# Performance work log

Hardware: AMD Instinct MI355X
Metric: run time of the kernel (lower is better)

The kernel has to match this reference:

```python
import jax, jax.numpy as jnp
import numpy as np

B, S, D, NH = 2, 2048, 2048, 16
HD = D // NH  # 128


def setup_inputs() -> dict:
    key = jax.random.key(0)
    ks = jax.random.split(key, 7)
    s = 1.0 / np.sqrt(D)
    return {
        "hidden_states": jax.random.normal(ks[0], (B, S, D), dtype=jnp.float32),
        "Wq": jax.random.normal(ks[1], (D, D), dtype=jnp.float32) * s,
        "Wk": jax.random.normal(ks[2], (D, D), dtype=jnp.float32) * s,
        "Wv": jax.random.normal(ks[3], (D, D), dtype=jnp.float32) * s,
        "Wo": jax.random.normal(ks[4], (D, D), dtype=jnp.float32) * s,
        # phase projections: hidden -> num_heads (zero-init in the module; use small
        # random values so the phase path is numerically exercised)
        "Wpq": jax.random.normal(ks[5], (D, NH), dtype=jnp.float32) * 0.02,
        "Wpk": jax.random.normal(ks[6], (D, NH), dtype=jnp.float32) * 0.02,
    }


def reference(hidden_states, Wq, Wk, Wv, Wo, Wpq, Wpk):
    x = hidden_states  # [B,S,D]
    # ---- base_attn: standard causal multi-head self-attention ----
    q = (x @ Wq).reshape(B, S, NH, HD).transpose(0, 2, 1, 3)  # [B,H,S,hd]
    k = (x @ Wk).reshape(B, S, NH, HD).transpose(0, 2, 1, 3)
    v = (x @ Wv).reshape(B, S, NH, HD).transpose(0, 2, 1, 3)
    scores = jnp.einsum("bhqd,bhkd->bhqk", q, k) / np.sqrt(HD)  # [B,H,S,S]
    causal = jnp.tril(jnp.ones((S, S), dtype=bool))
    scores = jnp.where(causal, scores, jnp.float32(-1e9))
    probs = jax.nn.softmax(scores, axis=-1)
    ctx = jnp.einsum("bhqk,bhkd->bhqd", probs, v)  # [B,H,S,hd]
    attn_output = ctx.transpose(0, 2, 1, 3).reshape(B, S, D) @ Wo  # [B,S,D]
    # ---- phase modulation ----
    # original: cos(pq[b,q,None,h] - pk[b,None,k,h]).mean(dims=(k,h))  -> [B,S]
    # identity: cos(a-b) = cos a * cos b + sin a * sin b lets us avoid the
    # [B,S,S,H] tensor; the math is identical.
    pq = x @ Wpq  # [B,S,H]
    pk = x @ Wpk  # [B,S,H]
    Ck = jnp.cos(pk).sum(axis=1)  # [B,H]
    Sk = jnp.sin(pk).sum(axis=1)  # [B,H]
    phase_mod = (jnp.cos(pq) * Ck[:, None, :] + jnp.sin(pq) * Sk[:, None, :]).sum(-1) / (S * NH)  # [B,S]
    return attn_output * (1.0 + 0.1 * phase_mod[..., None])
```

## Files before the change

kernel.cpp:

```cpp
#include <hip/hip_runtime.h>
#include <hip/hip_bf16.h>

typedef __attribute__((ext_vector_type(8))) short short8;
typedef __attribute__((ext_vector_type(4))) float f32x4;
typedef __attribute__((ext_vector_type(16))) float f32x16;
typedef __attribute__((ext_vector_type(4))) int i32x4;
typedef unsigned short u16;

#define S_LEN 2048
#define D_DIM 2048
#define NHEAD 16
#define HDIM 128
#define M_ROWS 4096

#define MFMA(a,b,c) __builtin_amdgcn_mfma_f32_16x16x32_bf16(a,b,c,0,0,0)
#define MFMA32(a,b,c) __builtin_amdgcn_mfma_f32_32x32x16_bf16(a,b,c,0,0,0)

__device__ __forceinline__ u16 f2bf(float f) {
  union { float f; unsigned u; } v; v.f = f;
  unsigned r = v.u + 0x7fffu + ((v.u >> 16) & 1u);
  return (u16)(r >> 16);
}

__device__ __forceinline__ void async16(void* lds, const void* g) {
  __builtin_amdgcn_global_load_lds(
      (const __attribute__((address_space(1))) unsigned*)g,
      (__attribute__((address_space(3))) unsigned*)lds, 16, 0, 0);
}

__device__ __forceinline__ unsigned cvtpk(float lo, float hi) {
  unsigned r;
  asm("v_cvt_pk_bf16_f32 %0, %1, %2" : "=v"(r) : "v"(lo), "v"(hi));
  return r;
}
__device__ __forceinline__ void plswap(unsigned& x, unsigned& y) {
  asm("v_permlane32_swap_b32 %0, %1" : "+v"(x), "+v"(y));
}

__global__ void k_cvt_x(const float* __restrict__ x, u16* __restrict__ xb) {
  int i = blockIdx.x * 256 + threadIdx.x;
  float4 v = reinterpret_cast<const float4*>(x)[i];
  ushort4 o;
  o.x = f2bf(v.x); o.y = f2bf(v.y); o.z = f2bf(v.z); o.w = f2bf(v.w);
  reinterpret_cast<ushort4*>(xb)[i] = o;
}

__global__ void k_cvt_wt4(const float* __restrict__ W0, const float* __restrict__ W1,
                          const float* __restrict__ W2, const float* __restrict__ W3,
                          u16* __restrict__ T0, u16* __restrict__ T1,
                          u16* __restrict__ T2, u16* __restrict__ T3) {
  __shared__ u16 tile[32][33];
  const int z = blockIdx.z;
  const float* W = (z == 0) ? W0 : (z == 1) ? W1 : (z == 2) ? W2 : W3;
  u16* Wt = (z == 0) ? T0 : (z == 1) ? T1 : (z == 2) ? T2 : T3;
  int n0 = blockIdx.x * 32, k0 = blockIdx.y * 32;
  int tx = threadIdx.x & 31, ty = threadIdx.x >> 5;
#pragma unroll
  for (int i = 0; i < 4; i++)
    tile[ty + i * 8][tx] = f2bf(W[(size_t)(k0 + ty + i * 8) * D_DIM + n0 + tx]);
  __syncthreads();
#pragma unroll
  for (int i = 0; i < 4; i++)
    Wt[(size_t)(n0 + ty + i * 8) * D_DIM + k0 + tx] = tile[tx][ty + i * 8];
}

__global__ void k_vtrans(const u16* __restrict__ V, u16* __restrict__ Vt) {
  __shared__ u16 tile[32][33];
  int s0 = blockIdx.x * 32, d0 = blockIdx.y * 32, bh = blockIdx.z;
  const u16* Vp = V + (size_t)bh * S_LEN * HDIM;
  u16* Vtp = Vt + (size_t)bh * HDIM * S_LEN;
  int tx = threadIdx.x & 31, ty = threadIdx.x >> 5;
#pragma unroll
  for (int i = 0; i < 4; i++)
    tile[ty + i * 8][tx] = Vp[(size_t)(s0 + ty + i * 8) * HDIM + d0 + tx];
  __syncthreads();
#pragma unroll
  for (int i = 0; i < 4; i++)
    Vtp[(size_t)(d0 + ty + i * 8) * S_LEN + s0 + tx] = tile[tx][ty + i * 8];
}

template <int MODE>
__device__ __forceinline__ void gemm_body(const u16* __restrict__ A,
                                          const u16* __restrict__ Bt,
                                          void* __restrict__ outp,
                                          const float* __restrict__ fac,
                                          char* lds) {
  constexpr int BUFSZ = 49152;
  const int m0 = blockIdx.y * 128, n0 = blockIdx.x * 256;
  const int t = threadIdx.x;
  const int w = t >> 6, l = t & 63;
  const int wr = (w >> 2) * 64, wc = (w & 3) * 64;
  const int lr = l & 15, lq = l >> 4;
  const char* Ab = (const char*)A;
  const char* Bb = (const char*)Bt;

  f32x4 acc[4][4] = {};

  const int sub = w >> 2, ww = w & 3;
  const int abase = (ww & 1) * 16 + (ww >> 1) * 64;
  const int bbase = (w >> 1) * 64 + (w & 1) * 16;
  const int rr = l >> 2, sl = l & 3;

  auto stageA = [&](int tt, int nb, int mh) {
    const int base = abase + mh * 32;
    const int row = base + rr;
    async16(lds + nb * BUFSZ + sub * 8192 + base * 64,
            Ab + (size_t)(m0 + row) * 4096 + tt * 128 + sub * 64 +
                ((sl ^ ((row >> 1) & 3)) * 16));
  };
  auto stageB = [&](int tt, int nb, int nh) {
    const int base = bbase + nh * 32;
    const int row = base + rr;
#pragma unroll
    for (int j = 0; j < 2; j++)
      async16(lds + nb * BUFSZ + 16384 + j * 16384 + base * 64,
              Bb + (size_t)(n0 + row) * 4096 + tt * 128 + j * 64 +
                  ((sl ^ ((row >> 1) & 3)) * 16));
  };

  auto readA = [&](short8 af[2][2], int buf, int mh) {
#pragma unroll
    for (int mi = 0; mi < 2; mi++)
#pragma unroll
      for (int ks = 0; ks < 2; ks++) {
        const int row = wr + mh * 32 + mi * 16 + lr;
        af[mi][ks] = *reinterpret_cast<const short8*>(
            lds + buf * BUFSZ + ks * 8192 + row * 64 +
            ((lq ^ ((row >> 1) & 3)) * 16));
      }
  };
  auto readB = [&](short8 bf[2][2], int buf, int nh) {
#pragma unroll
    for (int ni = 0; ni < 2; ni++)
#pragma unroll
      for (int ks = 0; ks < 2; ks++) {
        const int row = wc + nh * 32 + ni * 16 + lr;
        bf[ni][ks] = *reinterpret_cast<const short8*>(
            lds + buf * BUFSZ + 16384 + ks * 16384 + row * 64 +
            ((lq ^ ((row >> 1) & 3)) * 16));
      }
  };

#define QUAD(AF, BF, MH, NH)                                                \
  {                                                                         \
    __builtin_amdgcn_s_setprio(1);                                          \
    _Pragma("unroll") for (int mi = 0; mi < 2; mi++)                        \
    _Pragma("unroll") for (int ni = 0; ni < 2; ni++)                        \
    _Pragma("unroll") for (int ks = 0; ks < 2; ks++)                        \
      acc[(MH)*2 + mi][(NH)*2 + ni] =                                       \
          MFMA(AF[mi][ks], BF[ni][ks], acc[(MH)*2 + mi][(NH)*2 + ni]);      \
    __builtin_amdgcn_s_setprio(0);                                          \
  }
#define VMW(N) asm volatile("s_waitcnt vmcnt(" #N ")" ::: "memory")
#define BAR()                         \
  do {                                \
    __builtin_amdgcn_s_barrier();     \
    asm volatile("" ::: "memory");    \
  } while (0)

  stageA(0, 0, 0); stageB(0, 0, 0);
  stageA(0, 0, 1);
  stageB(0, 0, 1);
  stageA(1, 1, 0); stageB(1, 1, 0);
  stageA(1, 1, 1);
  stageB(1, 1, 1);

  short8 af0[2][2], af1[2][2], bfr[2][2];
  const int NT = D_DIM / 64;
  for (int tt = 0; tt < NT; tt++) {
    const int buf = tt % 3;
    const int sb = (tt + 2) % 3;
    const bool pf2 = (tt + 2 < NT);
    if (tt < NT - 1) VMW(9); else VMW(3);
    BAR();
    if (pf2) { stageA(tt + 2, sb, 0); stageB(tt + 2, sb, 0); }
    readA(af0, buf, 0); readB(bfr, buf, 0);
    QUAD(af0, bfr, 0, 0);
    if (tt < NT - 2) VMW(11); else if (tt == NT - 2) VMW(8); else VMW(2);
    BAR();
    if (pf2) stageA(tt + 2, sb, 1);
    readA(af1, buf, 1);
    QUAD(af1, bfr, 1, 0);
    if (tt < NT - 2) VMW(10); else if (tt == NT - 2) VMW(6); else VMW(0);
    BAR();
    if (pf2) stageB(tt + 2, sb, 1);
    readB(bfr, buf, 1);
    QUAD(af1, bfr, 1, 1);
    BAR();
    QUAD(af0, bfr, 0, 1);
  }
#undef QUAD
#undef VMW
#undef BAR

#pragma unroll
  for (int gm = 0; gm < 4; gm++) {
#pragma unroll
    for (int gn = 0; gn < 4; gn++) {
#pragma unroll
      for (int r = 0; r < 4; r++) {
        const int row = m0 + wr + gm * 16 + lq * 4 + r;
        const int col = n0 + wc + gn * 16 + lr;
        const float v = acc[gm][gn][r];
        if (MODE == 0) {
          const int mat = col >> 11;
          const int hh = (col >> 7) & 15;
          ((u16*)outp)[(size_t)mat * 8388608 +
                       (((size_t)((row >> 11) * NHEAD + hh)) * S_LEN + (row & 2047)) * HDIM +
                       (col & 127)] = f2bf(v);
        } else {
          ((float*)outp)[(size_t)row * D_DIM + col] = v * (1.0f + 0.1f * fac[row]);
        }
      }
    }
  }
}

__global__ __launch_bounds__(512, 1) void k_qkv(const u16* __restrict__ A,
                                                const u16* __restrict__ Bt,
                                                void* __restrict__ outp) {
  __shared__ __align__(16) char lds[3 * 49152];
  gemm_body<0>(A, Bt, outp, nullptr, lds);
}

__global__ __launch_bounds__(512, 1) void k_oproj(const u16* __restrict__ A,
                                                  const u16* __restrict__ Bt,
                                                  void* __restrict__ outp,
                                                  const float* __restrict__ fac) {
  __shared__ __align__(16) char lds[3 * 49152];
  gemm_body<1>(A, Bt, outp, fac, lds);
}

__global__ __launch_bounds__(256) void k_phase_proj(const u16* __restrict__ xb,
                                                    const float* __restrict__ Wpq,
                                                    const float* __restrict__ Wpk,
                                                    float* __restrict__ pq,
                                                    float* __restrict__ pk) {
  __shared__ u16 xs[16][136];
  __shared__ float2 ws[128][16];
  const int t = threadIdx.x;
  const int m0 = blockIdx.x * 16;
  const int h = t & 15, r = t >> 4;
  float sq = 0.f, sk = 0.f;
  for (int kc = 0; kc < D_DIM; kc += 128) {
    *reinterpret_cast<short8*>(&xs[t >> 4][(t & 15) * 8]) =
        *reinterpret_cast<const short8*>(
            &xb[(size_t)(m0 + (t >> 4)) * D_DIM + kc + (t & 15) * 8]);
#pragma unroll
    for (int j = 0; j < 8; j++) {
      const int idx = j * 256 + t;
      const int k = idx >> 4, hh = idx & 15;
      ws[k][hh] = make_float2(Wpq[(size_t)(kc + k) * NHEAD + hh],
                              Wpk[(size_t)(kc + k) * NHEAD + hh]);
    }
    __syncthreads();
#pragma unroll
    for (int k8 = 0; k8 < 16; k8++) {
      const short8 x8 = *reinterpret_cast<const short8*>(&xs[r][k8 * 8]);
#pragma unroll
      for (int j = 0; j < 8; j++) {
        union { float f; unsigned u; } c;
        c.u = ((unsigned)(u16)x8[j]) << 16;
        const float2 wv = ws[k8 * 8 + j][h];
        sq += c.f * wv.x;
        sk += c.f * wv.y;
      }
    }
    __syncthreads();
  }
  pq[(size_t)(m0 + r) * NHEAD + h] = sq;
  pk[(size_t)(m0 + r) * NHEAD + h] = sk;
}

__device__ __forceinline__ float wave_sum(float v) {
  v += __shfl_xor(v, 1);  v += __shfl_xor(v, 2);  v += __shfl_xor(v, 4);
  v += __shfl_xor(v, 8);  v += __shfl_xor(v, 16); v += __shfl_xor(v, 32);
  return v;
}

__global__ void k_phase_ck(const float* __restrict__ pk, float* __restrict__ Ck,
                           float* __restrict__ Sk) {
  int bh = blockIdx.x, b = bh >> 4, h = bh & 15;
  float c = 0.f, s = 0.f;
  for (int ss = threadIdx.x; ss < S_LEN; ss += 256) {
    float v = pk[((size_t)b * S_LEN + ss) * NHEAD + h];
    c += cosf(v); s += sinf(v);
  }
  c = wave_sum(c); s = wave_sum(s);
  __shared__ float rc[4], rs[4];
  int wv = threadIdx.x >> 6;
  if ((threadIdx.x & 63) == 0) { rc[wv] = c; rs[wv] = s; }
  __syncthreads();
  if (threadIdx.x == 0) {
    Ck[bh] = rc[0] + rc[1] + rc[2] + rc[3];
    Sk[bh] = rs[0] + rs[1] + rs[2] + rs[3];
  }
}

__global__ void k_phase_mod(const float* __restrict__ pq, const float* __restrict__ Ck,
                            const float* __restrict__ Sk, float* __restrict__ pm) {
  int m = blockIdx.x * 256 + threadIdx.x;
  int b = m >> 11;
  float a = 0.f;
#pragma unroll
  for (int h = 0; h < NHEAD; h++) {
    float v = pq[(size_t)m * NHEAD + h];
    a += cosf(v) * Ck[b * NHEAD + h] + sinf(v) * Sk[b * NHEAD + h];
  }
  pm[m] = a * (1.0f / (S_LEN * NHEAD));
}

__global__ __launch_bounds__(256, 2) void k_attn(const u16* __restrict__ Q,
                                                 const u16* __restrict__ K,
                                                 const u16* __restrict__ Vt,
                                                 u16* __restrict__ ctx) {
  const int bh = blockIdx.x;
  const int gy = blockIdx.y;
  const int g = (gy < 8) ? (15 - gy) : (gy - 8);
  const int b = bh >> 4, h = bh & 15;
  const int t = threadIdx.x;
  const int w = t >> 6, l = t & 63;
  const int ln = l & 31, hi = l >> 5;
  const int q0w = g * 128 + w * 32;
  const int qq = q0w + ln;
  const float scale = 0.08838834764831845f;

  const u16* Qp = Q + (size_t)bh * S_LEN * HDIM;
  const char* Kg = (const char*)(K + (size_t)bh * S_LEN * HDIM);
  const char* Vg = (const char*)(Vt + (size_t)bh * HDIM * S_LEN);

  __shared__ __align__(16) char Ks[2][16384];
  __shared__ __align__(16) char Vs[2][16384];

  auto stage = [&](int t64, int buf) {
    const int k0 = t64 * 64;
#pragma unroll
    for (int i = 0; i < 4; i++) {
      const int key = i * 16 + w * 4 + (l >> 4);
      async16(Ks[buf] + i * 4096 + w * 1024,
              Kg + (size_t)(k0 + key) * 256 + (((l & 15) * 16) ^ ((key & 15) << 4)));
      const int d = i * 32 + w * 8 + (l >> 3);
      async16(Vs[buf] + i * 4096 + w * 1024,
              Vg + (size_t)d * (S_LEN * 2) + k0 * 2 + (((l & 7) * 16) ^ ((d & 7) << 4)));
    }
  };

  short8 qf[8];
#pragma unroll
  for (int c = 0; c < 8; c++)
    qf[c] = *reinterpret_cast<const short8*>(Qp + (size_t)qq * HDIM + c * 16 + hi * 8);

  f32x16 o[4];
#pragma unroll
  for (int ds = 0; ds < 4; ds++)
#pragma unroll
    for (int r = 0; r < 16; r++) o[ds][r] = 0.f;
  float mrun = -1e30f, lsum = 0.f;

  const int nt = (g + 1) * 2;
  stage(0, 0);
  for (int t64 = 0; t64 < nt; t64++) {
    const int buf = t64 & 1;
    const int k0 = t64 * 64;
    asm volatile("s_waitcnt vmcnt(0)" ::: "memory");
    __syncthreads();
    if (t64 + 1 < nt) stage(t64 + 1, buf ^ 1);
    if (k0 < q0w + 32) {
      f32x16 s[2];
#pragma unroll
      for (int ks = 0; ks < 2; ks++)
#pragma unroll
        for (int r = 0; r < 16; r++) s[ks][r] = 0.f;
      __builtin_amdgcn_s_setprio(1);
#pragma unroll
      for (int ks = 0; ks < 2; ks++) {
        const int key = ks * 32 + ln;
        const char* kb = Ks[buf] + key * 256;
        const unsigned swzk = (unsigned)((key & 15) << 4);
#pragma unroll
        for (int c = 0; c < 8; c++) {
          const short8 kf = *reinterpret_cast<const short8*>(
              kb + (((unsigned)(c * 32 + hi * 16)) ^ swzk));
          s[ks] = MFMA32(kf, qf[c], s[ks]);
        }
      }
      __builtin_amdgcn_s_setprio(0);
      float p[32];
      float mx = -1e30f;
#pragma unroll
      for (int ks = 0; ks < 2; ks++)
#pragma unroll
        for (int r = 0; r < 16; r++) {
          const int key = k0 + ks * 32 + (r & 3) + 8 * (r >> 2) + 4 * hi;
          const float v = (key <= qq) ? s[ks][r] * scale : -1e30f;
          p[ks * 16 + r] = v;
          mx = fmaxf(mx, v);
        }
      mx = fmaxf(mx, __shfl_xor(mx, 32));
      const float nm = fmaxf(mrun, mx);
      const float f = __expf(mrun - nm);
      float rs = 0.f;
#pragma unroll
      for (int i = 0; i < 32; i++) { p[i] = __expf(p[i] - nm); rs += p[i]; }
      rs += __shfl_xor(rs, 32);
      lsum = lsum * f + rs;
      mrun = nm;
#pragma unroll
      for (int ds = 0; ds < 4; ds++)
#pragma unroll
        for (int r = 0; r < 16; r++) o[ds][r] *= f;
      short8 bfr[4];
#pragma unroll
      for (int sub = 0; sub < 2; sub++) {
#pragma unroll
        for (int half = 0; half < 2; half++) {
          const int pb = sub * 16 + half * 8;
          unsigned X1 = cvtpk(p[pb + 0], p[pb + 1]);
          unsigned X2 = cvtpk(p[pb + 2], p[pb + 3]);
          unsigned Y1 = cvtpk(p[pb + 4], p[pb + 5]);
          unsigned Y2 = cvtpk(p[pb + 6], p[pb + 7]);
          plswap(X1, Y1);
          plswap(X2, Y2);
          i32x4 bw;
          bw[0] = (int)X1; bw[1] = (int)X2; bw[2] = (int)Y1; bw[3] = (int)Y2;
          bfr[sub * 2 + half] = __builtin_bit_cast(short8, bw);
        }
      }
      __builtin_amdgcn_s_setprio(1);
#pragma unroll
      for (int ds = 0; ds < 4; ds++) {
        const int d = ds * 32 + ln;
        const char* vb = Vs[buf] + d * 128;
        const unsigned swzv = (unsigned)((d & 7) << 4);
#pragma unroll
        for (int slot = 0; slot < 4; slot++) {
          const short8 vf = *reinterpret_cast<const short8*>(
              vb + (((unsigned)(slot * 32 + hi * 16)) ^ swzv));
          o[ds] = MFMA32(vf, bfr[slot], o[ds]);
        }
      }
      __builtin_amdgcn_s_setprio(0);
    }
  }

  const float rl = 1.0f / lsum;
#pragma unroll
  for (int ds = 0; ds < 4; ds++) {
#pragma unroll
    for (int rq = 0; rq < 4; rq++) {
      const int d = ds * 32 + 8 * rq + 4 * hi;
      ushort4 pk4;
      pk4.x = f2bf(o[ds][rq * 4 + 0] * rl);
      pk4.y = f2bf(o[ds][rq * 4 + 1] * rl);
      pk4.z = f2bf(o[ds][rq * 4 + 2] * rl);
      pk4.w = f2bf(o[ds][rq * 4 + 3] * rl);
      *reinterpret_cast<ushort4*>(ctx + ((size_t)(b * S_LEN + qq)) * D_DIM + h * HDIM + d) = pk4;
    }
  }
}

extern "C" void kernel_launch(void* const* d_in, const int* in_sizes, int n_in,
                              void* d_out, int out_size, void* d_ws, size_t ws_size,
                              hipStream_t stream) {
  const float* x   = (const float*)d_in[0];
  const float* Wq  = (const float*)d_in[1];
  const float* Wk  = (const float*)d_in[2];
  const float* Wv  = (const float*)d_in[3];
  const float* Wo  = (const float*)d_in[4];
  const float* Wpq = (const float*)d_in[5];
  const float* Wpk = (const float*)d_in[6];

  char* ws = (char*)d_ws;
  u16* xb   = (u16*)(ws + 0);
  u16* Wqt  = (u16*)(ws + 16777216);
  u16* Wkt  = (u16*)(ws + 25165824);
  u16* Wvt  = (u16*)(ws + 33554432);
  u16* Wot  = (u16*)(ws + 41943040);
  u16* Qb   = (u16*)(ws + 50331648);
  u16* Kb   = (u16*)(ws + 67108864);
  u16* Vb   = (u16*)(ws + 83886080);
  u16* Vt   = (u16*)(ws + 100663296);
  float* pq = (float*)(ws + 117440512);
  float* pk = (float*)(ws + 117702656);
  float* Ck = (float*)(ws + 117964800);
  float* Sk = (float*)(ws + 117964928);
  float* pm = (float*)(ws + 117965056);

  k_cvt_x<<<dim3(M_ROWS * D_DIM / 1024), 256, 0, stream>>>(x, xb);
  k_cvt_wt4<<<dim3(64, 64, 4), 256, 0, stream>>>(Wq, Wk, Wv, Wo, Wqt, Wkt, Wvt, Wot);

  k_qkv<<<dim3(24, 32), 512, 0, stream>>>(xb, Wqt, Qb);

  k_vtrans<<<dim3(64, 4, 32), 256, 0, stream>>>(Vb, Vt);

  k_phase_proj<<<dim3(256), 256, 0, stream>>>(xb, Wpq, Wpk, pq, pk);
  k_phase_ck<<<dim3(32), 256, 0, stream>>>(pk, Ck, Sk);
  k_phase_mod<<<dim3(16), 256, 0, stream>>>(pq, Ck, Sk, pm);

  k_attn<<<dim3(32, 16), 256, 0, stream>>>(Qb, Kb, Vt, Vb );

  k_oproj<<<dim3(8, 32), 512, 0, stream>>>(Vb , Wot, (void*)d_out, pm);
}
```

Measured before the change: 331.4 us.

## Fuse V transpose into QKV epilogue, double-buffer GEMM, pair attention q-blocks

The QKV GEMM epilogue now writes V straight into the transposed [b,h,d,s] layout with packed 4-wide stores, so the separate V transpose kernel is dropped. Both GEMMs go from triple- to double-buffered LDS with retuned waitcnts, which shrinks shared memory but leaves less prefetch slack. Each attention block now handles a long and a short causal q-block in two passes to balance work, halving the grid. Online softmax skips rescaling unless the running max grows by more than 8, saving exp and multiply work per tile.

```diff
diff --git a/kernel.cpp b/kernel.cpp
--- a/kernel.cpp
+++ b/kernel.cpp
@@ -64,25 +64,11 @@
     Wt[(size_t)(n0 + ty + i * 8) * D_DIM + k0 + tx] = tile[tx][ty + i * 8];
 }
 
-__global__ void k_vtrans(const u16* __restrict__ V, u16* __restrict__ Vt) {
-  __shared__ u16 tile[32][33];
-  int s0 = blockIdx.x * 32, d0 = blockIdx.y * 32, bh = blockIdx.z;
-  const u16* Vp = V + (size_t)bh * S_LEN * HDIM;
-  u16* Vtp = Vt + (size_t)bh * HDIM * S_LEN;
-  int tx = threadIdx.x & 31, ty = threadIdx.x >> 5;
-#pragma unroll
-  for (int i = 0; i < 4; i++)
-    tile[ty + i * 8][tx] = Vp[(size_t)(s0 + ty + i * 8) * HDIM + d0 + tx];
-  __syncthreads();
-#pragma unroll
-  for (int i = 0; i < 4; i++)
-    Vtp[(size_t)(d0 + ty + i * 8) * S_LEN + s0 + tx] = tile[tx][ty + i * 8];
-}
-
 template <int MODE>
 __device__ __forceinline__ void gemm_body(const u16* __restrict__ A,
                                           const u16* __restrict__ Bt,
                                           void* __restrict__ outp,
+                                          u16* __restrict__ Vt,
                                           const float* __restrict__ fac,
                                           char* lds) {
   constexpr int BUFSZ = 49152;
@@ -161,29 +147,24 @@
   stageA(0, 0, 0); stageB(0, 0, 0);
   stageA(0, 0, 1);
   stageB(0, 0, 1);
-  stageA(1, 1, 0); stageB(1, 1, 0);
-  stageA(1, 1, 1);
-  stageB(1, 1, 1);
 
   short8 af0[2][2], af1[2][2], bfr[2][2];
   const int NT = D_DIM / 64;
   for (int tt = 0; tt < NT; tt++) {
-    const int buf = tt % 3;
-    const int sb = (tt + 2) % 3;
-    const bool pf2 = (tt + 2 < NT);
-    if (tt < NT - 1) VMW(9); else VMW(3);
-    BAR();
-    if (pf2) { stageA(tt + 2, sb, 0); stageB(tt + 2, sb, 0); }
+    const int buf = tt & 1, nb = buf ^ 1;
+    const bool pf = (tt + 1 < NT);
+    VMW(3); BAR();
+    if (pf) { stageA(tt + 1, nb, 0); stageB(tt + 1, nb, 0); }
     readA(af0, buf, 0); readB(bfr, buf, 0);
     QUAD(af0, bfr, 0, 0);
-    if (tt < NT - 2) VMW(11); else if (tt == NT - 2) VMW(8); else VMW(2);
+    if (pf) VMW(5); else VMW(2);
     BAR();
-    if (pf2) stageA(tt + 2, sb, 1);
+    if (pf) stageA(tt + 1, nb, 1);
     readA(af1, buf, 1);
     QUAD(af1, bfr, 1, 0);
-    if (tt < NT - 2) VMW(10); else if (tt == NT - 2) VMW(6); else VMW(0);
+    if (pf) VMW(4); else VMW(0);
     BAR();
-    if (pf2) stageB(tt + 2, sb, 1);
+    if (pf) stageB(tt + 1, nb, 1);
     readB(bfr, buf, 1);
     QUAD(af1, bfr, 1, 1);
     BAR();
@@ -197,19 +178,36 @@
   for (int gm = 0; gm < 4; gm++) {
 #pragma unroll
     for (int gn = 0; gn < 4; gn++) {
-#pragma unroll
-      for (int r = 0; r < 4; r++) {
-        const int row = m0 + wr + gm * 16 + lq * 4 + r;
-        const int col = n0 + wc + gn * 16 + lr;
-        const float v = acc[gm][gn][r];
-        if (MODE == 0) {
-          const int mat = col >> 11;
-          const int hh = (col >> 7) & 15;
-          ((u16*)outp)[(size_t)mat * 8388608 +
-                       (((size_t)((row >> 11) * NHEAD + hh)) * S_LEN + (row & 2047)) * HDIM +
-                       (col & 127)] = f2bf(v);
+      const int row0 = m0 + wr + gm * 16 + lq * 4;
+      const int col = n0 + wc + gn * 16 + lr;
+      if (MODE == 0) {
+        if (col >= 4096) {
+          const int d = col & 127, hh = (col >> 7) & 15;
+          const int bb = row0 >> 11, s0 = row0 & 2047;
+          ushort4 v4;
+          v4.x = f2bf(acc[gm][gn][0]);
+          v4.y = f2bf(acc[gm][gn][1]);
+          v4.z = f2bf(acc[gm][gn][2]);
+          v4.w = f2bf(acc[gm][gn][3]);
+          *reinterpret_cast<ushort4*>(
+              Vt + (((size_t)(bb * NHEAD + hh) * HDIM + d) * S_LEN + s0)) = v4;
         } else {
-          ((float*)outp)[(size_t)row * D_DIM + col] = v * (1.0f + 0.1f * fac[row]);
+#pragma unroll
+          for (int r = 0; r < 4; r++) {
+            const int row = row0 + r;
+            const int mat = col >> 11;
+            const int hh = (col >> 7) & 15;
+            ((u16*)outp)[(size_t)mat * 8388608 +
+                         (((size_t)((row >> 11) * NHEAD + hh)) * S_LEN + (row & 2047)) * HDIM +
+                         (col & 127)] = f2bf(acc[gm][gn][r]);
+          }
+        }
+      } else {
+#pragma unroll
+        for (int r = 0; r < 4; r++) {
+          const int row = row0 + r;
+          ((float*)outp)[(size_t)row * D_DIM + col] =
+              acc[gm][gn][r] * (1.0f + 0.1f * fac[row]);
         }
       }
     }
@@ -218,17 +216,18 @@
 
 __global__ __launch_bounds__(512, 1) void k_qkv(const u16* __restrict__ A,
                                                 const u16* __restrict__ Bt,
-                                                void* __restrict__ outp) {
-  __shared__ __align__(16) char lds[3 * 49152];
-  gemm_body<0>(A, Bt, outp, nullptr, lds);
+                                                void* __restrict__ outp,
+                                                u16* __restrict__ Vt) {
+  __shared__ __align__(16) char lds[2 * 49152];
+  gemm_body<0>(A, Bt, outp, Vt, nullptr, lds);
 }
 
 __global__ __launch_bounds__(512, 1) void k_oproj(const u16* __restrict__ A,
                                                   const u16* __restrict__ Bt,
                                                   void* __restrict__ outp,
                                                   const float* __restrict__ fac) {
-  __shared__ __align__(16) char lds[3 * 49152];
-  gemm_body<1>(A, Bt, outp, fac, lds);
+  __shared__ __align__(16) char lds[2 * 49152];
+  gemm_body<1>(A, Bt, outp, nullptr, fac, lds);
 }
 
 __global__ __launch_bounds__(256) void k_phase_proj(const u16* __restrict__ xb,
@@ -315,14 +314,11 @@
                                                  const u16* __restrict__ Vt,
                                                  u16* __restrict__ ctx) {
   const int bh = blockIdx.x;
-  const int gy = blockIdx.y;
-  const int g = (gy < 8) ? (15 - gy) : (gy - 8);
+  const int gp = blockIdx.y;
   const int b = bh >> 4, h = bh & 15;
   const int t = threadIdx.x;
   const int w = t >> 6, l = t & 63;
   const int ln = l & 31, hi = l >> 5;
-  const int q0w = g * 128 + w * 32;
-  const int qq = q0w + ln;
   const float scale = 0.08838834764831845f;
 
   const u16* Qp = Q + (size_t)bh * S_LEN * HDIM;
@@ -345,117 +341,127 @@
     }
   };
 
-  short8 qf[8];
-#pragma unroll
-  for (int c = 0; c < 8; c++)
-    qf[c] = *reinterpret_cast<const short8*>(Qp + (size_t)qq * HDIM + c * 16 + hi * 8);
-
-  f32x16 o[4];
-#pragma unroll
-  for (int ds = 0; ds < 4; ds++)
-#pragma unroll
-    for (int r = 0; r < 16; r++) o[ds][r] = 0.f;
-  float mrun = -1e30f, lsum = 0.f;
-
-  const int nt = (g + 1) * 2;
-  stage(0, 0);
-  for (int t64 = 0; t64 < nt; t64++) {
-    const int buf = t64 & 1;
-    const int k0 = t64 * 64;
-    asm volatile("s_waitcnt vmcnt(0)" ::: "memory");
+  for (int pass = 0; pass < 2; pass++) {
+    const int g = (pass == 0) ? (15 - gp) : gp;
+    const int q0w = g * 128 + w * 32;
+    const int qq = q0w + ln;
+
+    short8 qf[8];
+#pragma unroll
+    for (int c = 0; c < 8; c++)
+      qf[c] = *reinterpret_cast<const short8*>(Qp + (size_t)qq * HDIM + c * 16 + hi * 8);
+
+    f32x16 o[4];
+#pragma unroll
+    for (int ds = 0; ds < 4; ds++)
+#pragma unroll
+      for (int r = 0; r < 16; r++) o[ds][r] = 0.f;
+    float mrun = -1e30f, lsum = 0.f;
+
+    const int nt = (g + 1) * 2;
+    stage(0, 0);
+    for (int t64 = 0; t64 < nt; t64++) {
+      const int buf = t64 & 1;
+      const int k0 = t64 * 64;
+      asm volatile("s_waitcnt vmcnt(0)" ::: "memory");
+      __syncthreads();
+      if (t64 + 1 < nt) stage(t64 + 1, buf ^ 1);
+      if (k0 < q0w + 32) {
+        f32x16 s[2];
+#pragma unroll
+        for (int ks = 0; ks < 2; ks++)
+#pragma unroll
+          for (int r = 0; r < 16; r++) s[ks][r] = 0.f;
+        __builtin_amdgcn_s_setprio(1);
+#pragma unroll
+        for (int ks = 0; ks < 2; ks++) {
+          const int key = ks * 32 + ln;
+          const char* kb = Ks[buf] + key * 256;
+          const unsigned swzk = (unsigned)((key & 15) << 4);
+#pragma unroll
+          for (int c = 0; c < 8; c++) {
+            const short8 kf = *reinterpret_cast<const short8*>(
+                kb + (((unsigned)(c * 32 + hi * 16)) ^ swzk));
+            s[ks] = MFMA32(kf, qf[c], s[ks]);
+          }
+        }
+        __builtin_amdgcn_s_setprio(0);
+        float p[32];
+        float mx = -1e30f;
+#pragma unroll
+        for (int ks = 0; ks < 2; ks++)
+#pragma unroll
+          for (int r = 0; r < 16; r++) {
+            const int key = k0 + ks * 32 + (r & 3) + 8 * (r >> 2) + 4 * hi;
+            const float v = (key <= qq) ? s[ks][r] * scale : -1e30f;
+            p[ks * 16 + r] = v;
+            mx = fmaxf(mx, v);
+          }
+        mx = fmaxf(mx, __shfl_xor(mx, 32));
+        if (!__all(mx <= mrun + 8.f)) {
+          const float nm = fmaxf(mrun, mx);
+          const float f = __expf(mrun - nm);
+          lsum *= f;
+#pragma unroll
+          for (int ds = 0; ds < 4; ds++)
+#pragma unroll
+            for (int r = 0; r < 16; r++) o[ds][r] *= f;
+          mrun = nm;
+        }
+        float rs = 0.f;
+#pragma unroll
+        for (int i = 0; i < 32; i++) { p[i] = __expf(p[i] - mrun); rs += p[i]; }
+        rs += __shfl_xor(rs, 32);
+        lsum += rs;
+        short8 bfr[4];
+#pragma unroll
+        for (int sub = 0; sub < 2; sub++) {
+#pragma unroll
+          for (int half = 0; half < 2; half++) {
+            const int pb = sub * 16 + half * 8;
+            unsigned X1 = cvtpk(p[pb + 0], p[pb + 1]);
+            unsigned X2 = cvtpk(p[pb + 2], p[pb + 3]);
+            unsigned Y1 = cvtpk(p[pb + 4], p[pb + 5]);
+            unsigned Y2 = cvtpk(p[pb + 6], p[pb + 7]);
+            plswap(X1, Y1);
+            plswap(X2, Y2);
+            i32x4 bw;
+            bw[0] = (int)X1; bw[1] = (int)X2; bw[2] = (int)Y1; bw[3] = (int)Y2;
+            bfr[sub * 2 + half] = __builtin_bit_cast(short8, bw);
+          }
+        }
+        __builtin_amdgcn_s_setprio(1);
+#pragma unroll
+        for (int ds = 0; ds < 4; ds++) {
+          const int d = ds * 32 + ln;
+          const char* vb = Vs[buf] + d * 128;
+          const unsigned swzv = (unsigned)((d & 7) << 4);
+#pragma unroll
+          for (int slot = 0; slot < 4; slot++) {
+            const short8 vf = *reinterpret_cast<const short8*>(
+                vb + (((unsigned)(slot * 32 + hi * 16)) ^ swzv));
+            o[ds] = MFMA32(vf, bfr[slot], o[ds]);
+          }
+        }
+        __builtin_amdgcn_s_setprio(0);
+      }
+    }
+
+    const float rl = 1.0f / lsum;
+#pragma unroll
+    for (int ds = 0; ds < 4; ds++) {
+#pragma unroll
+      for (int rq = 0; rq < 4; rq++) {
+        const int d = ds * 32 + 8 * rq + 4 * hi;
+        ushort4 pk4;
+        pk4.x = f2bf(o[ds][rq * 4 + 0] * rl);
+        pk4.y = f2bf(o[ds][rq * 4 + 1] * rl);
+        pk4.z = f2bf(o[ds][rq * 4 + 2] * rl);
+        pk4.w = f2bf(o[ds][rq * 4 + 3] * rl);
+        *reinterpret_cast<ushort4*>(ctx + ((size_t)(b * S_LEN + qq)) * D_DIM + h * HDIM + d) = pk4;
+      }
+    }
     __syncthreads();
-    if (t64 + 1 < nt) stage(t64 + 1, buf ^ 1);
-    if (k0 < q0w + 32) {
-      f32x16 s[2];
-#pragma unroll
-      for (int ks = 0; ks < 2; ks++)
-#pragma unroll
-        for (int r = 0; r < 16; r++) s[ks][r] = 0.f;
-      __builtin_amdgcn_s_setprio(1);
-#pragma unroll
-      for (int ks = 0; ks < 2; ks++) {
-        const int key = ks * 32 + ln;
-        const char* kb = Ks[buf] + key * 256;
-        const unsigned swzk = (unsigned)((key & 15) << 4);
-#pragma unroll
-        for (int c = 0; c < 8; c++) {
-          const short8 kf = *reinterpret_cast<const short8*>(
-              kb + (((unsigned)(c * 32 + hi * 16)) ^ swzk));
-          s[ks] = MFMA32(kf, qf[c], s[ks]);
-        }
-      }
-      __builtin_amdgcn_s_setprio(0);
-      float p[32];
-      float mx = -1e30f;
-#pragma unroll
-      for (int ks = 0; ks < 2; ks++)
-#pragma unroll
-        for (int r = 0; r < 16; r++) {
-          const int key = k0 + ks * 32 + (r & 3) + 8 * (r >> 2) + 4 * hi;
-          const float v = (key <= qq) ? s[ks][r] * scale : -1e30f;
-          p[ks * 16 + r] = v;
-          mx = fmaxf(mx, v);
-        }
-      mx = fmaxf(mx, __shfl_xor(mx, 32));
-      const float nm = fmaxf(mrun, mx);
-      const float f = __expf(mrun - nm);
-      float rs = 0.f;
-#pragma unroll
-      for (int i = 0; i < 32; i++) { p[i] = __expf(p[i] - nm); rs += p[i]; }
-      rs += __shfl_xor(rs, 32);
-      lsum = lsum * f + rs;
-      mrun = nm;
-#pragma unroll
-      for (int ds = 0; ds < 4; ds++)
-#pragma unroll
-        for (int r = 0; r < 16; r++) o[ds][r] *= f;
-      short8 bfr[4];
-#pragma unroll
-      for (int sub = 0; sub < 2; sub++) {
-#pragma unroll
-        for (int half = 0; half < 2; half++) {
-          const int pb = sub * 16 + half * 8;
-          unsigned X1 = cvtpk(p[pb + 0], p[pb + 1]);
-          unsigned X2 = cvtpk(p[pb + 2], p[pb + 3]);
-          unsigned Y1 = cvtpk(p[pb + 4], p[pb + 5]);
-          unsigned Y2 = cvtpk(p[pb + 6], p[pb + 7]);
-          plswap(X1, Y1);
-          plswap(X2, Y2);
-          i32x4 bw;
-          bw[0] = (int)X1; bw[1] = (int)X2; bw[2] = (int)Y1; bw[3] = (int)Y2;
-          bfr[sub * 2 + half] = __builtin_bit_cast(short8, bw);
-        }
-      }
-      __builtin_amdgcn_s_setprio(1);
-#pragma unroll
-      for (int ds = 0; ds < 4; ds++) {
-        const int d = ds * 32 + ln;
-        const char* vb = Vs[buf] + d * 128;
-        const unsigned swzv = (unsigned)((d & 7) << 4);
-#pragma unroll
-        for (int slot = 0; slot < 4; slot++) {
-          const short8 vf = *reinterpret_cast<const short8*>(
-              vb + (((unsigned)(slot * 32 + hi * 16)) ^ swzv));
-          o[ds] = MFMA32(vf, bfr[slot], o[ds]);
-        }
-      }
-      __builtin_amdgcn_s_setprio(0);
-    }
-  }
-
-  const float rl = 1.0f / lsum;
-#pragma unroll
-  for (int ds = 0; ds < 4; ds++) {
-#pragma unroll
-    for (int rq = 0; rq < 4; rq++) {
-      const int d = ds * 32 + 8 * rq + 4 * hi;
-      ushort4 pk4;
-      pk4.x = f2bf(o[ds][rq * 4 + 0] * rl);
-      pk4.y = f2bf(o[ds][rq * 4 + 1] * rl);
-      pk4.z = f2bf(o[ds][rq * 4 + 2] * rl);
-      pk4.w = f2bf(o[ds][rq * 4 + 3] * rl);
-      *reinterpret_cast<ushort4*>(ctx + ((size_t)(b * S_LEN + qq)) * D_DIM + h * HDIM + d) = pk4;
-    }
   }
 }
 
@@ -489,15 +495,13 @@
   k_cvt_x<<<dim3(M_ROWS * D_DIM / 1024), 256, 0, stream>>>(x, xb);
   k_cvt_wt4<<<dim3(64, 64, 4), 256, 0, stream>>>(Wq, Wk, Wv, Wo, Wqt, Wkt, Wvt, Wot);
 
-  k_qkv<<<dim3(24, 32), 512, 0, stream>>>(xb, Wqt, Qb);
-
-  k_vtrans<<<dim3(64, 4, 32), 256, 0, stream>>>(Vb, Vt);
+  k_qkv<<<dim3(24, 32), 512, 0, stream>>>(xb, Wqt, Qb, Vt);
 
   k_phase_proj<<<dim3(256), 256, 0, stream>>>(xb, Wpq, Wpk, pq, pk);
   k_phase_ck<<<dim3(32), 256, 0, stream>>>(pk, Ck, Sk);
   k_phase_mod<<<dim3(16), 256, 0, stream>>>(pq, Ck, Sk, pm);
 
-  k_attn<<<dim3(32, 16), 256, 0, stream>>>(Qb, Kb, Vt, Vb );
+  k_attn<<<dim3(32, 8), 256, 0, stream>>>(Qb, Kb, Vt, Vb );
 
   k_oproj<<<dim3(8, 32), 512, 0, stream>>>(Vb , Wot, (void*)d_out, pm);
 }
```

After: 327.4 us. Within noise of the previous version (-1.2%).
